# Kernel tuning notes

Measured on AMD Instinct MI355X. Metric: run time of the kernel, lower is better.

The kernel has to match this reference:

```python
import jax, jax.numpy as jnp
import numpy as np

D_MODEL = 1024
NUM_HEADS = 16


def setup_inputs() -> dict:
    key = jax.random.key(0)
    k1, k2, k3, k4, k5 = jax.random.split(key, 5)
    b, n, d = 4, 2048, D_MODEL
    s = 1.0 / np.sqrt(d)
    x = jax.random.normal(k1, (b, n, d), dtype=jnp.float32)
    v_w = jax.random.uniform(k2, (d, d), dtype=jnp.float32, minval=-s, maxval=s)  # Linear weight [out,in]
    v_b = jax.random.uniform(k3, (d,), dtype=jnp.float32, minval=-s, maxval=s)
    o_w = jax.random.uniform(k4, (d, d), dtype=jnp.float32, minval=-s, maxval=s)
    o_b = jax.random.uniform(k5, (d,), dtype=jnp.float32, minval=-s, maxval=s)
    return {"x": x, "v_w": v_w, "v_b": v_b, "o_w": o_w, "o_b": o_b}


def reference(x, v_w, v_b, o_w, o_b):
    b, n, d = x.shape
    h = NUM_HEADS
    dh = d // h
    # shared QKV projection: q = k = v
    v = jnp.einsum('bnd,ed->bne', x, v_w) + v_b            # [b,n,d]
    v = v.reshape(b, n, h, dh).transpose(0, 2, 1, 3)        # [b,h,n,dh]
    scale = 1.0 / jnp.sqrt(jnp.asarray(dh, dtype=x.dtype))
    scores = jnp.einsum('bhnd,bhmd->bhnm', v, v) * scale    # [b,h,n,n]
    attn = jax.nn.softmax(scores, axis=-1)
    out = jnp.einsum('bhnm,bhmd->bhnd', attn, v)            # [b,h,n,dh]
    out = out.transpose(0, 2, 1, 3).reshape(b, n, d)        # concat heads
    return jnp.einsum('bnd,ed->bne', out, o_w) + o_b
```

## Files before the change

kernel.cpp:

```cpp
#include <hip/hip_runtime.h>
#include <stdint.h>

typedef __attribute__((ext_vector_type(8))) short short8;
typedef __attribute__((ext_vector_type(4))) float f32x4;
typedef __attribute__((ext_vector_type(4))) unsigned int u32x4;
typedef __attribute__((ext_vector_type(2))) unsigned int u32x2;

#define MFMA16(a, b, c) __builtin_amdgcn_mfma_f32_16x16x32_bf16((a), (b), (c), 0, 0, 0)

#define GLD_LDS16(g, l)                                                                  \
    __builtin_amdgcn_global_load_lds((const __attribute__((address_space(1))) void*)(g), \
                                     (__attribute__((address_space(3))) void*)(l), 16, 0, 0)

#if defined(__has_builtin)
#if __has_builtin(__builtin_amdgcn_exp2f)
#define FAST_EXP2(x) __builtin_amdgcn_exp2f(x)
#endif
#endif
#ifndef FAST_EXP2
__device__ __forceinline__ float fast_exp2_asm(float x) {
    float r;
    asm volatile("v_exp_f32 %0, %1\ns_nop 1" : "=v"(r) : "v"(x));
    return r;
}
#define FAST_EXP2(x) fast_exp2_asm(x)
#endif

#if defined(__has_builtin)
#if __has_builtin(__builtin_amdgcn_permlane32_swap) && __has_builtin(__builtin_amdgcn_permlane16_swap)
#define HAVE_PERMLANE_SWAP 1
#endif
#endif

__device__ __forceinline__ void permlane_regroup(unsigned int& x, unsigned int& y) {
#ifdef HAVE_PERMLANE_SWAP
    {
        auto r = __builtin_amdgcn_permlane32_swap(x, y, false, false);
        auto r2 = __builtin_amdgcn_permlane16_swap(r[0], r[1], false, false);
        x = r2[0];
        y = r2[1];
    }
#else
    asm volatile(
        "s_nop 3\n\t"
        "v_permlane32_swap_b32 %0, %1\n\t"
        "s_nop 3\n\t"
        "v_permlane16_swap_b32 %0, %1\n\t"
        "s_nop 3"
        : "+v"(x), "+v"(y));
#endif
}

__device__ __forceinline__ float bf2f(unsigned short u) {
    unsigned int x = ((unsigned int)u) << 16;
    float f;
    __builtin_memcpy(&f, &x, 4);
    return f;
}
__device__ __forceinline__ unsigned short f2bf(float f) {
    unsigned int x;
    __builtin_memcpy(&x, &f, 4);
    unsigned int r = x + 0x7FFFu + ((x >> 16) & 1u);
    return (unsigned short)(r >> 16);
}
__device__ __forceinline__ unsigned int pack2bf(float a, float b) {
    unsigned int ua, ub;
    __builtin_memcpy(&ua, &a, 4);
    __builtin_memcpy(&ub, &b, 4);
    return __builtin_amdgcn_perm(ub + 0x8000u, ua + 0x8000u, 0x07060302u);
}
__device__ __forceinline__ unsigned int cvtpk_bf16(float a, float b) {
    unsigned int r;
    asm("v_cvt_pk_bf16_f32 %0, %1, %2\n\ts_nop 1" : "=v"(r) : "v"(a), "v"(b));
    return r;
}
__device__ __forceinline__ u32x4 cvt8(const float* p) {
    f32x4 g0 = *(const f32x4*)p;
    f32x4 g1 = *(const f32x4*)(p + 4);
    u32x4 r;
    r.x = pack2bf(g0[0], g0[1]);
    r.y = pack2bf(g0[2], g0[3]);
    r.z = pack2bf(g1[0], g1[1]);
    r.w = pack2bf(g1[2], g1[3]);
    return r;
}

__global__ __launch_bounds__(256) void cvt3_kernel(const float* __restrict__ a,
                                                   unsigned short* __restrict__ oa, int na8,
                                                   const float* __restrict__ b,
                                                   unsigned short* __restrict__ ob, int nb8,
                                                   const float* __restrict__ c,
                                                   unsigned short* __restrict__ oc, int nc8) {
    int i = blockIdx.x * 256 + threadIdx.x;
    if (i < na8) {
        *(u32x4*)(oa + (size_t)i * 8) = cvt8(a + (size_t)i * 8);
    } else if (i < na8 + nb8) {
        int j = i - na8;
        *(u32x4*)(ob + (size_t)j * 8) = cvt8(b + (size_t)j * 8);
    } else if (i < na8 + nb8 + nc8) {
        int j = i - na8 - nb8;
        *(u32x4*)(oc + (size_t)j * 8) = cvt8(c + (size_t)j * 8);
    }
}

template <int MODE>
__global__ __launch_bounds__(256) void gemm_dma_kernel(
    const unsigned short* __restrict__ A, const unsigned short* __restrict__ B,
    const float* __restrict__ bias, void* __restrict__ Cv, int M, int N, int K) {
    __shared__ __align__(16) unsigned short As[2][2][128 * 32];
    __shared__ __align__(16) unsigned short Bs[2][2][128 * 32];

    const int tid = threadIdx.x;
    const int wave = tid >> 6, lane = tid & 63;
    const int l15 = lane & 15, quad = lane >> 4;
    const int m0 = blockIdx.x * 128, n0 = blockIdx.y * 128;
    const int wm = (wave >> 1) * 64, wn = (wave & 1) * 64;

    const int row0 = tid >> 2, c0 = (tid & 3) * 8;
    const unsigned short* Ag0 = A + (size_t)(m0 + row0) * K + c0;
    const unsigned short* Ag1 = A + (size_t)(m0 + row0 + 64) * K + c0;
    const unsigned short* Bg0 = B + (size_t)(n0 + row0) * K + c0;
    const unsigned short* Bg1 = B + (size_t)(n0 + row0 + 64) * K + c0;
    const int wl = wave * 512;

#define STAGE(s, k0)                                     \
    do {                                                 \
        GLD_LDS16(Ag0 + (k0), &As[s][0][wl]);            \
        GLD_LDS16(Ag1 + (k0), &As[s][0][2048 + wl]);     \
        GLD_LDS16(Ag0 + (k0) + 32, &As[s][1][wl]);       \
        GLD_LDS16(Ag1 + (k0) + 32, &As[s][1][2048 + wl]); \
        GLD_LDS16(Bg0 + (k0), &Bs[s][0][wl]);            \
        GLD_LDS16(Bg1 + (k0), &Bs[s][0][2048 + wl]);     \
        GLD_LDS16(Bg0 + (k0) + 32, &Bs[s][1][wl]);       \
        GLD_LDS16(Bg1 + (k0) + 32, &Bs[s][1][2048 + wl]); \
    } while (0)

    f32x4 acc[4][4];
#pragma unroll
    for (int i = 0; i < 4; i++)
#pragma unroll
        for (int j = 0; j < 4; j++) {
            f32x4 z = {0.f, 0.f, 0.f, 0.f};
            acc[i][j] = z;
        }

    STAGE(0, 0);
    for (int k0 = 0; k0 < K; k0 += 64) {
        const int s = (k0 >> 6) & 1;
        __syncthreads();
        if (k0 + 64 < K) STAGE(s ^ 1, k0 + 64);

        short8 a0[4], a1[4], b0[4], b1[4];
#pragma unroll
        for (int mt = 0; mt < 4; mt++) {
            a0[mt] = *(const short8*)&As[s][0][(wm + mt * 16 + l15) * 32 + quad * 8];
            a1[mt] = *(const short8*)&As[s][1][(wm + mt * 16 + l15) * 32 + quad * 8];
        }
#pragma unroll
        for (int nt = 0; nt < 4; nt++) {
            b0[nt] = *(const short8*)&Bs[s][0][(wn + nt * 16 + l15) * 32 + quad * 8];
            b1[nt] = *(const short8*)&Bs[s][1][(wn + nt * 16 + l15) * 32 + quad * 8];
        }
#pragma unroll
        for (int mt = 0; mt < 4; mt++)
#pragma unroll
            for (int nt = 0; nt < 4; nt++) acc[mt][nt] = MFMA16(a0[mt], b0[nt], acc[mt][nt]);
#pragma unroll
        for (int mt = 0; mt < 4; mt++)
#pragma unroll
            for (int nt = 0; nt < 4; nt++) acc[mt][nt] = MFMA16(a1[mt], b1[nt], acc[mt][nt]);
    }
#undef STAGE

    float bv[4];
#pragma unroll
    for (int nt = 0; nt < 4; nt++) bv[nt] = bias[n0 + wn + nt * 16 + l15];

#pragma unroll
    for (int mt = 0; mt < 4; mt++)
#pragma unroll
        for (int nt = 0; nt < 4; nt++)
#pragma unroll
            for (int i = 0; i < 4; i++) {
                int m = m0 + wm + mt * 16 + quad * 4 + i;
                int n = n0 + wn + nt * 16 + l15;
                float val = acc[mt][nt][i] + bv[nt];
                if (MODE == 0) {
                    int bb = m >> 11, ns = m & 2047, h = n >> 6, c = n & 63;
                    ((unsigned short*)Cv)[(size_t)(bb * 16 + h) * 131072 + (size_t)ns * 64 + c] =
                        f2bf(val);
                } else {
                    ((float*)Cv)[(size_t)m * N + n] = val;
                }
            }
}

template <bool AF32, bool BF32, int MODE>
__global__ __launch_bounds__(256) void gemm_bias_kernel(
    const void* __restrict__ Av, const void* __restrict__ Bv,
    const float* __restrict__ bias, void* __restrict__ Cv, int M, int N, int K) {
    __shared__ __align__(16) unsigned short As[128][40];
    __shared__ __align__(16) unsigned short Bs[128][40];

    const int tid = threadIdx.x;
    const int wave = tid >> 6, lane = tid & 63;
    const int l15 = lane & 15, quad = lane >> 4;
    const int m0 = blockIdx.x * 128, n0 = blockIdx.y * 128;
    const int wm = (wave >> 1) * 64, wn = (wave & 1) * 64;

    f32x4 acc[4][4];
#pragma unroll
    for (int i = 0; i < 4; i++)
#pragma unroll
        for (int j = 0; j < 4; j++) {
            f32x4 z = {0.f, 0.f, 0.f, 0.f};
            acc[i][j] = z;
        }

    for (int k0 = 0; k0 < K; k0 += 32) {
        __syncthreads();
#pragma unroll
        for (int rep = 0; rep < 2; rep++) {
            int chunk = tid + rep * 256;
            int row = chunk >> 2, c8 = (chunk & 3) * 8;
            if (AF32) {
                const float* Af = (const float*)Av;
                *(u32x4*)&As[row][c8] = cvt8(&Af[(size_t)(m0 + row) * K + k0 + c8]);
            } else {
                const unsigned short* Ab = (const unsigned short*)Av;
                *(f32x4*)&As[row][c8] = *(const f32x4*)&Ab[(size_t)(m0 + row) * K + k0 + c8];
            }
            if (BF32) {
                const float* Bf = (const float*)Bv;
                *(u32x4*)&Bs[row][c8] = cvt8(&Bf[(size_t)(n0 + row) * K + k0 + c8]);
            } else {
                const unsigned short* Bb = (const unsigned short*)Bv;
                *(f32x4*)&Bs[row][c8] = *(const f32x4*)&Bb[(size_t)(n0 + row) * K + k0 + c8];
            }
        }
        __syncthreads();

        short8 a[4], b[4];
#pragma unroll
        for (int mt = 0; mt < 4; mt++) a[mt] = *(const short8*)&As[wm + mt * 16 + l15][quad * 8];
#pragma unroll
        for (int nt = 0; nt < 4; nt++) b[nt] = *(const short8*)&Bs[wn + nt * 16 + l15][quad * 8];
#pragma unroll
        for (int mt = 0; mt < 4; mt++)
#pragma unroll
            for (int nt = 0; nt < 4; nt++) acc[mt][nt] = MFMA16(a[mt], b[nt], acc[mt][nt]);
    }

    float bv[4];
#pragma unroll
    for (int nt = 0; nt < 4; nt++) bv[nt] = bias[n0 + wn + nt * 16 + l15];

#pragma unroll
    for (int mt = 0; mt < 4; mt++)
#pragma unroll
        for (int nt = 0; nt < 4; nt++)
#pragma unroll
            for (int i = 0; i < 4; i++) {
                int m = m0 + wm + mt * 16 + quad * 4 + i;
                int n = n0 + wn + nt * 16 + l15;
                float val = acc[mt][nt][i] + bv[nt];
                if (MODE == 0) {
                    int bb = m >> 11, ns = m & 2047, h = n >> 6, c = n & 63;
                    ((unsigned short*)Cv)[(size_t)(bb * 16 + h) * 131072 + (size_t)ns * 64 + c] =
                        f2bf(val);
                } else {
                    ((float*)Cv)[(size_t)m * N + n] = val;
                }
            }
}

__global__ __launch_bounds__(256) void transpose_kernel(const unsigned short* __restrict__ V,
                                                        unsigned short* __restrict__ Vt) {
    __shared__ __align__(16) unsigned short T[64][72];
    const int tid = threadIdx.x;
    const int n0 = blockIdx.x * 64;
    const size_t base = (size_t)blockIdx.y * 131072;
#pragma unroll
    for (int rep = 0; rep < 2; rep++) {
        int chunk = tid + rep * 256;
        int row = chunk >> 3, c8 = (chunk & 7) * 8;
        *(short8*)&T[row][c8] = *(const short8*)&V[base + (size_t)(n0 + row) * 64 + c8];
    }
    __syncthreads();
#pragma unroll
    for (int rep = 0; rep < 2; rep++) {
        int chunk = tid + rep * 256;
        int d = chunk >> 3, n8 = (chunk & 7) * 8;
        short8 o;
#pragma unroll
        for (int j = 0; j < 8; j++) o[j] = (short)T[n8 + j][d];
        *(short8*)&Vt[base + (size_t)d * 2048 + n0 + n8] = o;
    }
}

__global__ __launch_bounds__(256, 4) void attn_kernel(const unsigned short* __restrict__ V,
                                                      const unsigned short* __restrict__ Vt,
                                                      unsigned short* __restrict__ O) {
    __shared__ __align__(16) unsigned short Ks[2][64 * 64];
    __shared__ __align__(16) unsigned short VTs[2][64 * 64];

    const int tid = threadIdx.x;
    const int wave = tid >> 6, lane = tid & 63;
    const int l15 = lane & 15, quad = lane >> 4;
    const int sx = l15 & 7;

    const int flat = blockIdx.y * 16 + blockIdx.x;
    const int bh = (flat & 7) * 8 + ((flat >> 3) & 7);
    const int q0 = (flat >> 6) * 128;

    const unsigned short* Vh = V + (size_t)bh * 131072;
    const unsigned short* VhT = Vt + (size_t)bh * 131072;
    const int wm = wave * 32;

    const int srow = wave * 16 + (lane >> 3);
    const int scol = ((lane & 7) ^ (lane >> 3)) * 8;
    const unsigned short* gK = Vh + (size_t)srow * 64 + scol;
    const unsigned short* gVT = VhT + (size_t)srow * 2048 + scol;

#define KSTAGE(s, kv)                                                       \
    do {                                                                    \
        GLD_LDS16(gK + (size_t)(kv) * 64, &Ks[s][wave * 1024]);             \
        GLD_LDS16(gK + (size_t)(kv) * 64 + 512, &Ks[s][wave * 1024 + 512]); \
    } while (0)
#define VSTAGE(s, kv)                                                 \
    do {                                                              \
        GLD_LDS16(gVT + (kv), &VTs[s][wave * 1024]);                  \
        GLD_LDS16(gVT + (kv) + 8 * 2048, &VTs[s][wave * 1024 + 512]); \
    } while (0)

    KSTAGE(0, 0);
    VSTAGE(0, 0);

    short8 bq[2][2];
#pragma unroll
    for (int mt = 0; mt < 2; mt++)
#pragma unroll
        for (int ks = 0; ks < 2; ks++) {
            short8 g = *(const short8*)&Vh[(size_t)(q0 + wm + mt * 16 + l15) * 64 + ks * 32 +
                                           quad * 8];
            u32x4 a;
            a.x = cvtpk_bf16(bf2f((unsigned short)g[0]) * 0.1803368801f,
                             bf2f((unsigned short)g[1]) * 0.1803368801f);
            a.y = cvtpk_bf16(bf2f((unsigned short)g[2]) * 0.1803368801f,
                             bf2f((unsigned short)g[3]) * 0.1803368801f);
            a.z = cvtpk_bf16(bf2f((unsigned short)g[4]) * 0.1803368801f,
                             bf2f((unsigned short)g[5]) * 0.1803368801f);
            a.w = cvtpk_bf16(bf2f((unsigned short)g[6]) * 0.1803368801f,
                             bf2f((unsigned short)g[7]) * 0.1803368801f);
            bq[mt][ks] = *(short8*)&a;
        }

    short8 vones;
#pragma unroll
    for (int j = 0; j < 8; j++) vones[j] = (short)0x3F80;

    f32x4 oacc[2][4];
    f32x4 lsacc[2];
#pragma unroll
    for (int mt = 0; mt < 2; mt++) {
        f32x4 z = {0.f, 0.f, 0.f, 0.f};
        lsacc[mt] = z;
#pragma unroll
        for (int ct = 0; ct < 4; ct++) oacc[mt][ct] = z;
    }

    for (int kv0 = 0; kv0 < 2048; kv0 += 64) {
        const int s = (kv0 >> 6) & 1;
        __syncthreads();
        if (kv0 + 64 < 2048) {
            KSTAGE(s ^ 1, kv0 + 64);
            VSTAGE(s ^ 1, kv0 + 64);
        }

        f32x4 st[4][2];
#pragma unroll
        for (int nt = 0; nt < 4; nt++) {
            const int krow = (nt * 16 + l15) * 64;
            short8 ak0 = *(const short8*)&Ks[s][krow + ((quad ^ sx) << 3)];
            short8 ak1 = *(const short8*)&Ks[s][krow + (((4 | quad) ^ sx) << 3)];
#pragma unroll
            for (int mt = 0; mt < 2; mt++) {
                f32x4 z = {0.f, 0.f, 0.f, 0.f};
                z = MFMA16(ak0, bq[mt][0], z);
                z = MFMA16(ak1, bq[mt][1], z);
                st[nt][mt] = z;
            }
        }

        short8 ap[2][2];
#pragma unroll
        for (int mt = 0; mt < 2; mt++) {
            unsigned int w[4][2];
#pragma unroll
            for (int nt = 0; nt < 4; nt++) {
                f32x4 p;
#pragma unroll
                for (int i = 0; i < 4; i++) p[i] = FAST_EXP2(st[nt][mt][i]);
                w[nt][0] = cvtpk_bf16(p[0], p[1]);
                w[nt][1] = cvtpk_bf16(p[2], p[3]);
            }
#pragma unroll
            for (int kt = 0; kt < 2; kt++) {
                unsigned int x0 = w[2 * kt][0], x1 = w[2 * kt][1];
                unsigned int y0 = w[2 * kt + 1][0], y1 = w[2 * kt + 1][1];
                permlane_regroup(x0, y0);
                permlane_regroup(x1, y1);
                u32x4 a;
                a.x = x0;
                a.y = x1;
                a.z = y0;
                a.w = y1;
                ap[mt][kt] = *(short8*)&a;
            }
        }

#pragma unroll
        for (int kt = 0; kt < 2; kt++) {
#pragma unroll
            for (int ct = 0; ct < 4; ct++) {
                short8 bvf =
                    *(const short8*)&VTs[s][(ct * 16 + l15) * 64 + ((((kt << 2) | quad) ^ sx) << 3)];
#pragma unroll
                for (int mt = 0; mt < 2; mt++) oacc[mt][ct] = MFMA16(ap[mt][kt], bvf, oacc[mt][ct]);
            }
#pragma unroll
            for (int mt = 0; mt < 2; mt++) lsacc[mt] = MFMA16(ap[mt][kt], vones, lsacc[mt]);
        }
    }
#undef KSTAGE
#undef VSTAGE

    float inv[2][4];
#pragma unroll
    for (int mt = 0; mt < 2; mt++)
#pragma unroll
        for (int i = 0; i < 4; i++) inv[mt][i] = 1.0f / lsacc[mt][i];

    const int bb = bh >> 4, h = bh & 15;
#pragma unroll
    for (int mt = 0; mt < 2; mt++)
#pragma unroll
        for (int i = 0; i < 4; i++) {
            int m = q0 + wm + mt * 16 + quad * 4 + i;
            size_t rowbase = ((size_t)(bb * 2048 + m)) * 1024 + h * 64;
#pragma unroll
            for (int ct = 0; ct < 4; ct++)
                O[rowbase + ct * 16 + l15] = f2bf(oacc[mt][ct][i] * inv[mt][i]);
        }
}

extern "C" void kernel_launch(void* const* d_in, const int* in_sizes, int n_in, void* d_out,
                              int out_size, void* d_ws, size_t ws_size, hipStream_t stream) {
    (void)in_sizes; (void)n_in; (void)out_size;
    const float* x = (const float*)d_in[0];
    const float* v_w = (const float*)d_in[1];
    const float* v_b = (const float*)d_in[2];
    const float* o_w = (const float*)d_in[3];
    const float* o_b = (const float*)d_in[4];
    float* out = (float*)d_out;

    unsigned short* Vbuf = (unsigned short*)d_out;
    unsigned short* Vtbuf = Vbuf + (size_t)8192 * 1024;
    unsigned short* Obuf = (unsigned short*)d_ws;

    const size_t need =
        ((size_t)8192 * 1024  + (size_t)8192 * 1024  + 2 * (size_t)1024 * 1024) * 2;
    if (ws_size >= need) {
        unsigned short* xbf = Obuf + (size_t)8192 * 1024;
        unsigned short* wv = xbf + (size_t)8192 * 1024;
        unsigned short* wo = wv + (size_t)1024 * 1024;
        cvt3_kernel<<<5120, 256, 0, stream>>>(x, xbf, 1048576, v_w, wv, 131072, o_w, wo, 131072);
        gemm_dma_kernel<0><<<dim3(64, 8), 256, 0, stream>>>(xbf, wv, v_b, Vbuf, 8192, 1024, 1024);
        transpose_kernel<<<dim3(32, 64), 256, 0, stream>>>(Vbuf, Vtbuf);
        attn_kernel<<<dim3(16, 64), 256, 0, stream>>>(Vbuf, Vtbuf, Obuf);
        gemm_dma_kernel<1><<<dim3(64, 8), 256, 0, stream>>>(Obuf, wo, o_b, out, 8192, 1024, 1024);
    } else {
        gemm_bias_kernel<true, true, 0>
            <<<dim3(64, 8), 256, 0, stream>>>(x, v_w, v_b, Vbuf, 8192, 1024, 1024);
        transpose_kernel<<<dim3(32, 64), 256, 0, stream>>>(Vbuf, Vtbuf);
        attn_kernel<<<dim3(16, 64), 256, 0, stream>>>(Vbuf, Vtbuf, Obuf);
        gemm_bias_kernel<false, true, 1>
            <<<dim3(64, 8), 256, 0, stream>>>(Obuf, o_w, o_b, out, 8192, 1024, 1024);
    }
}
```

Baseline: 217.6 us.

## Halve attention query tile per block and remap GEMM blocks for XCD locality

```diff
diff --git a/kernel.cpp b/kernel.cpp
--- a/kernel.cpp
+++ b/kernel.cpp
@@ -113,7 +113,10 @@
     const int tid = threadIdx.x;
     const int wave = tid >> 6, lane = tid & 63;
     const int l15 = lane & 15, quad = lane >> 4;
-    const int m0 = blockIdx.x * 128, n0 = blockIdx.y * 128;
+    const int id = blockIdx.y * gridDim.x + blockIdx.x;
+    const int xcd = id & 7;
+    const int p = id >> 3;
+    const int m0 = (xcd * 8 + (p >> 3)) * 128, n0 = (p & 7) * 128;
     const int wm = (wave >> 1) * 64, wn = (wave & 1) * 64;
 
     const int row0 = tid >> 2, c0 = (tid & 3) * 8;
@@ -298,7 +301,7 @@
     }
 }
 
-__global__ __launch_bounds__(256, 4) void attn_kernel(const unsigned short* __restrict__ V,
+__global__ __launch_bounds__(256, 5) void attn_kernel(const unsigned short* __restrict__ V,
                                                       const unsigned short* __restrict__ Vt,
                                                       unsigned short* __restrict__ O) {
     __shared__ __align__(16) unsigned short Ks[2][64 * 64];
@@ -309,13 +312,13 @@
     const int l15 = lane & 15, quad = lane >> 4;
     const int sx = l15 & 7;
 
-    const int flat = blockIdx.y * 16 + blockIdx.x;
+    const int flat = blockIdx.y * 32 + blockIdx.x;
     const int bh = (flat & 7) * 8 + ((flat >> 3) & 7);
-    const int q0 = (flat >> 6) * 128;
+    const int q0 = (flat >> 6) * 64;
 
     const unsigned short* Vh = V + (size_t)bh * 131072;
     const unsigned short* VhT = Vt + (size_t)bh * 131072;
-    const int wm = wave * 32;
+    const int wm = wave * 16;
 
     const int srow = wave * 16 + (lane >> 3);
     const int scol = ((lane & 7) ^ (lane >> 3)) * 8;
@@ -336,37 +339,33 @@
     KSTAGE(0, 0);
     VSTAGE(0, 0);
 
-    short8 bq[2][2];
-#pragma unroll
-    for (int mt = 0; mt < 2; mt++)
-#pragma unroll
-        for (int ks = 0; ks < 2; ks++) {
-            short8 g = *(const short8*)&Vh[(size_t)(q0 + wm + mt * 16 + l15) * 64 + ks * 32 +
-                                           quad * 8];
-            u32x4 a;
-            a.x = cvtpk_bf16(bf2f((unsigned short)g[0]) * 0.1803368801f,
-                             bf2f((unsigned short)g[1]) * 0.1803368801f);
-            a.y = cvtpk_bf16(bf2f((unsigned short)g[2]) * 0.1803368801f,
-                             bf2f((unsigned short)g[3]) * 0.1803368801f);
-            a.z = cvtpk_bf16(bf2f((unsigned short)g[4]) * 0.1803368801f,
-                             bf2f((unsigned short)g[5]) * 0.1803368801f);
-            a.w = cvtpk_bf16(bf2f((unsigned short)g[6]) * 0.1803368801f,
-                             bf2f((unsigned short)g[7]) * 0.1803368801f);
-            bq[mt][ks] = *(short8*)&a;
-        }
+    short8 bq[2];
+#pragma unroll
+    for (int ks = 0; ks < 2; ks++) {
+        short8 g = *(const short8*)&Vh[(size_t)(q0 + wm + l15) * 64 + ks * 32 + quad * 8];
+        u32x4 a;
+        a.x = cvtpk_bf16(bf2f((unsigned short)g[0]) * 0.1803368801f,
+                         bf2f((unsigned short)g[1]) * 0.1803368801f);
+        a.y = cvtpk_bf16(bf2f((unsigned short)g[2]) * 0.1803368801f,
+                         bf2f((unsigned short)g[3]) * 0.1803368801f);
+        a.z = cvtpk_bf16(bf2f((unsigned short)g[4]) * 0.1803368801f,
+                         bf2f((unsigned short)g[5]) * 0.1803368801f);
+        a.w = cvtpk_bf16(bf2f((unsigned short)g[6]) * 0.1803368801f,
+                         bf2f((unsigned short)g[7]) * 0.1803368801f);
+        bq[ks] = *(short8*)&a;
+    }
 
     short8 vones;
 #pragma unroll
     for (int j = 0; j < 8; j++) vones[j] = (short)0x3F80;
 
-    f32x4 oacc[2][4];
-    f32x4 lsacc[2];
-#pragma unroll
-    for (int mt = 0; mt < 2; mt++) {
+    f32x4 oacc[4];
+    f32x4 lsacc;
+    {
         f32x4 z = {0.f, 0.f, 0.f, 0.f};
-        lsacc[mt] = z;
-#pragma unroll
-        for (int ct = 0; ct < 4; ct++) oacc[mt][ct] = z;
+        lsacc = z;
+#pragma unroll
+        for (int ct = 0; ct < 4; ct++) oacc[ct] = z;
     }
 
     for (int kv0 = 0; kv0 < 2048; kv0 += 64) {
@@ -377,46 +376,40 @@
             VSTAGE(s ^ 1, kv0 + 64);
         }
 
-        f32x4 st[4][2];
+        f32x4 st[4];
 #pragma unroll
         for (int nt = 0; nt < 4; nt++) {
             const int krow = (nt * 16 + l15) * 64;
             short8 ak0 = *(const short8*)&Ks[s][krow + ((quad ^ sx) << 3)];
             short8 ak1 = *(const short8*)&Ks[s][krow + (((4 | quad) ^ sx) << 3)];
-#pragma unroll
-            for (int mt = 0; mt < 2; mt++) {
-                f32x4 z = {0.f, 0.f, 0.f, 0.f};
-                z = MFMA16(ak0, bq[mt][0], z);
-                z = MFMA16(ak1, bq[mt][1], z);
-                st[nt][mt] = z;
-            }
-        }
-
-        short8 ap[2][2];
-#pragma unroll
-        for (int mt = 0; mt < 2; mt++) {
-            unsigned int w[4][2];
-#pragma unroll
-            for (int nt = 0; nt < 4; nt++) {
-                f32x4 p;
-#pragma unroll
-                for (int i = 0; i < 4; i++) p[i] = FAST_EXP2(st[nt][mt][i]);
-                w[nt][0] = cvtpk_bf16(p[0], p[1]);
-                w[nt][1] = cvtpk_bf16(p[2], p[3]);
-            }
-#pragma unroll
-            for (int kt = 0; kt < 2; kt++) {
-                unsigned int x0 = w[2 * kt][0], x1 = w[2 * kt][1];
-                unsigned int y0 = w[2 * kt + 1][0], y1 = w[2 * kt + 1][1];
-                permlane_regroup(x0, y0);
-                permlane_regroup(x1, y1);
-                u32x4 a;
-                a.x = x0;
-                a.y = x1;
-                a.z = y0;
-                a.w = y1;
-                ap[mt][kt] = *(short8*)&a;
-            }
+            f32x4 z = {0.f, 0.f, 0.f, 0.f};
+            z = MFMA16(ak0, bq[0], z);
+            z = MFMA16(ak1, bq[1], z);
+            st[nt] = z;
+        }
+
+        unsigned int w[4][2];
+#pragma unroll
+        for (int nt = 0; nt < 4; nt++) {
+            f32x4 p;
+#pragma unroll
+            for (int i = 0; i < 4; i++) p[i] = FAST_EXP2(st[nt][i]);
+            w[nt][0] = cvtpk_bf16(p[0], p[1]);
+            w[nt][1] = cvtpk_bf16(p[2], p[3]);
+        }
+        short8 ap[2];
+#pragma unroll
+        for (int kt = 0; kt < 2; kt++) {
+            unsigned int x0 = w[2 * kt][0], x1 = w[2 * kt][1];
+            unsigned int y0 = w[2 * kt + 1][0], y1 = w[2 * kt + 1][1];
+            permlane_regroup(x0, y0);
+            permlane_regroup(x1, y1);
+            u32x4 a;
+            a.x = x0;
+            a.y = x1;
+            a.z = y0;
+            a.w = y1;
+            ap[kt] = *(short8*)&a;
         }
 
 #pragma unroll
@@ -425,33 +418,27 @@
             for (int ct = 0; ct < 4; ct++) {
                 short8 bvf =
                     *(const short8*)&VTs[s][(ct * 16 + l15) * 64 + ((((kt << 2) | quad) ^ sx) << 3)];
-#pragma unroll
-                for (int mt = 0; mt < 2; mt++) oacc[mt][ct] = MFMA16(ap[mt][kt], bvf, oacc[mt][ct]);
+                oacc[ct] = MFMA16(ap[kt], bvf, oacc[ct]);
             }
-#pragma unroll
-            for (int mt = 0; mt < 2; mt++) lsacc[mt] = MFMA16(ap[mt][kt], vones, lsacc[mt]);
+            lsacc = MFMA16(ap[kt], vones, lsacc);
         }
     }
 #undef KSTAGE
 #undef VSTAGE
 
-    float inv[2][4];
-#pragma unroll
-    for (int mt = 0; mt < 2; mt++)
-#pragma unroll
-        for (int i = 0; i < 4; i++) inv[mt][i] = 1.0f / lsacc[mt][i];
+    float inv[4];
+#pragma unroll
+    for (int i = 0; i < 4; i++) inv[i] = 1.0f / lsacc[i];
 
     const int bb = bh >> 4, h = bh & 15;
 #pragma unroll
-    for (int mt = 0; mt < 2; mt++)
-#pragma unroll
-        for (int i = 0; i < 4; i++) {
-            int m = q0 + wm + mt * 16 + quad * 4 + i;
-            size_t rowbase = ((size_t)(bb * 2048 + m)) * 1024 + h * 64;
-#pragma unroll
-            for (int ct = 0; ct < 4; ct++)
-                O[rowbase + ct * 16 + l15] = f2bf(oacc[mt][ct][i] * inv[mt][i]);
-        }
+    for (int i = 0; i < 4; i++) {
+        int m = q0 + wm + quad * 4 + i;
+        size_t rowbase = ((size_t)(bb * 2048 + m)) * 1024 + h * 64;
+#pragma unroll
+        for (int ct = 0; ct < 4; ct++)
+            O[rowbase + ct * 16 + l15] = f2bf(oacc[ct][i] * inv[i]);
+    }
 }
 
 extern "C" void kernel_launch(void* const* d_in, const int* in_sizes, int n_in, void* d_out,
@@ -477,13 +464,13 @@
         cvt3_kernel<<<5120, 256, 0, stream>>>(x, xbf, 1048576, v_w, wv, 131072, o_w, wo, 131072);
         gemm_dma_kernel<0><<<dim3(64, 8), 256, 0, stream>>>(xbf, wv, v_b, Vbuf, 8192, 1024, 1024);
         transpose_kernel<<<dim3(32, 64), 256, 0, stream>>>(Vbuf, Vtbuf);
-        attn_kernel<<<dim3(16, 64), 256, 0, stream>>>(Vbuf, Vtbuf, Obuf);
+        attn_kernel<<<dim3(32, 64), 256, 0, stream>>>(Vbuf, Vtbuf, Obuf);
         gemm_dma_kernel<1><<<dim3(64, 8), 256, 0, stream>>>(Obuf, wo, o_b, out, 8192, 1024, 1024);
     } else {
         gemm_bias_kernel<true, true, 0>
             <<<dim3(64, 8), 256, 0, stream>>>(x, v_w, v_b, Vbuf, 8192, 1024, 1024);
         transpose_kernel<<<dim3(32, 64), 256, 0, stream>>>(Vbuf, Vtbuf);
-        attn_kernel<<<dim3(16, 64), 256, 0, stream>>>(Vbuf, Vtbuf, Obuf);
+        attn_kernel<<<dim3(32, 64), 256, 0, stream>>>(Vbuf, Vtbuf, Obuf);
         gemm_bias_kernel<false, true, 1>
             <<<dim3(64, 8), 256, 0, stream>>>(Obuf, o_w, o_b, out, 8192, 1024, 1024);
     }
```

Measured after the change: 234.5 us. 1.08x slower.

## Swizzle GEMM LDS layout and remap blocks per XCD for L2 reuse

Applied to the files above, without the earlier changes.

```diff
diff --git a/kernel.cpp b/kernel.cpp
--- a/kernel.cpp
+++ b/kernel.cpp
@@ -107,32 +107,35 @@
 __global__ __launch_bounds__(256) void gemm_dma_kernel(
     const unsigned short* __restrict__ A, const unsigned short* __restrict__ B,
     const float* __restrict__ bias, void* __restrict__ Cv, int M, int N, int K) {
-    __shared__ __align__(16) unsigned short As[2][2][128 * 32];
-    __shared__ __align__(16) unsigned short Bs[2][2][128 * 32];
+    __shared__ __align__(16) unsigned short As[2][128 * 64];
+    __shared__ __align__(16) unsigned short Bs[2][128 * 64];
 
     const int tid = threadIdx.x;
     const int wave = tid >> 6, lane = tid & 63;
     const int l15 = lane & 15, quad = lane >> 4;
-    const int m0 = blockIdx.x * 128, n0 = blockIdx.y * 128;
+    const int sx = l15 & 7;
+    const int id = blockIdx.y * gridDim.x + blockIdx.x;
+    const int xcd = id & 7;
+    const int p = id >> 3;
+    const int m0 = (xcd * 8 + (p >> 3)) * 128, n0 = (p & 7) * 128;
     const int wm = (wave >> 1) * 64, wn = (wave & 1) * 64;
 
-    const int row0 = tid >> 2, c0 = (tid & 3) * 8;
-    const unsigned short* Ag0 = A + (size_t)(m0 + row0) * K + c0;
-    const unsigned short* Ag1 = A + (size_t)(m0 + row0 + 64) * K + c0;
-    const unsigned short* Bg0 = B + (size_t)(n0 + row0) * K + c0;
-    const unsigned short* Bg1 = B + (size_t)(n0 + row0 + 64) * K + c0;
-    const int wl = wave * 512;
-
-#define STAGE(s, k0)                                     \
-    do {                                                 \
-        GLD_LDS16(Ag0 + (k0), &As[s][0][wl]);            \
-        GLD_LDS16(Ag1 + (k0), &As[s][0][2048 + wl]);     \
-        GLD_LDS16(Ag0 + (k0) + 32, &As[s][1][wl]);       \
-        GLD_LDS16(Ag1 + (k0) + 32, &As[s][1][2048 + wl]); \
-        GLD_LDS16(Bg0 + (k0), &Bs[s][0][wl]);            \
-        GLD_LDS16(Bg1 + (k0), &Bs[s][0][2048 + wl]);     \
-        GLD_LDS16(Bg0 + (k0) + 32, &Bs[s][1][wl]);       \
-        GLD_LDS16(Bg1 + (k0) + 32, &Bs[s][1][2048 + wl]); \
+    const int srow = wave * 32 + (lane >> 3);
+    const int scol = ((lane & 7) ^ (lane >> 3)) * 8;
+    const unsigned short* Ag = A + (size_t)(m0 + srow) * K + scol;
+    const unsigned short* Bg = B + (size_t)(n0 + srow) * K + scol;
+    const int wl = wave * 2048;
+
+#define STAGE(s, k0)                                       \
+    do {                                                   \
+        GLD_LDS16(Ag + (k0), &As[s][wl]);                  \
+        GLD_LDS16(Ag + (k0) + 8 * K, &As[s][wl + 512]);    \
+        GLD_LDS16(Ag + (k0) + 16 * K, &As[s][wl + 1024]);  \
+        GLD_LDS16(Ag + (k0) + 24 * K, &As[s][wl + 1536]);  \
+        GLD_LDS16(Bg + (k0), &Bs[s][wl]);                  \
+        GLD_LDS16(Bg + (k0) + 8 * K, &Bs[s][wl + 512]);    \
+        GLD_LDS16(Bg + (k0) + 16 * K, &Bs[s][wl + 1024]);  \
+        GLD_LDS16(Bg + (k0) + 24 * K, &Bs[s][wl + 1536]);  \
     } while (0)
 
     f32x4 acc[4][4];
@@ -153,13 +156,15 @@
         short8 a0[4], a1[4], b0[4], b1[4];
 #pragma unroll
         for (int mt = 0; mt < 4; mt++) {
-            a0[mt] = *(const short8*)&As[s][0][(wm + mt * 16 + l15) * 32 + quad * 8];
-            a1[mt] = *(const short8*)&As[s][1][(wm + mt * 16 + l15) * 32 + quad * 8];
+            const int row = (wm + mt * 16 + l15) * 64;
+            a0[mt] = *(const short8*)&As[s][row + ((quad ^ sx) << 3)];
+            a1[mt] = *(const short8*)&As[s][row + (((4 | quad) ^ sx) << 3)];
         }
 #pragma unroll
         for (int nt = 0; nt < 4; nt++) {
-            b0[nt] = *(const short8*)&Bs[s][0][(wn + nt * 16 + l15) * 32 + quad * 8];
-            b1[nt] = *(const short8*)&Bs[s][1][(wn + nt * 16 + l15) * 32 + quad * 8];
+            const int row = (wn + nt * 16 + l15) * 64;
+            b0[nt] = *(const short8*)&Bs[s][row + ((quad ^ sx) << 3)];
+            b1[nt] = *(const short8*)&Bs[s][row + (((4 | quad) ^ sx) << 3)];
         }
 #pragma unroll
         for (int mt = 0; mt < 4; mt++)
```

After: 215.4 us. No clear change (-1.0%).
